# Optimization experiments

Measured on AMD Instinct MI355X. Metric: run time of the kernel, lower is better.

The kernel has to match this reference:

```python
import jax, jax.numpy as jnp
import numpy as np

D_MODEL = 1024
NUM_HEADS = 16
HEAD_DIM = D_MODEL // NUM_HEADS


def setup_inputs() -> dict:
    key = jax.random.key(0)
    ks = jax.random.split(key, 11)
    B, N = 2, 2048
    s = 1.0 / np.sqrt(D_MODEL)
    return {
        "query": jax.random.normal(ks[0], (B, N, D_MODEL), jnp.float32),
        "key":   jax.random.normal(ks[1], (B, N, D_MODEL), jnp.float32),
        "value": jax.random.normal(ks[2], (B, N, D_MODEL), jnp.float32),
        "Wq": jax.random.normal(ks[3], (D_MODEL, D_MODEL), jnp.float32) * s,
        "bq": jax.random.normal(ks[4], (D_MODEL,), jnp.float32) * 0.01,
        "Wk": jax.random.normal(ks[5], (D_MODEL, D_MODEL), jnp.float32) * s,
        "bk": jax.random.normal(ks[6], (D_MODEL,), jnp.float32) * 0.01,
        "Wv": jax.random.normal(ks[7], (D_MODEL, D_MODEL), jnp.float32) * s,
        "bv": jax.random.normal(ks[8], (D_MODEL,), jnp.float32) * 0.01,
        "Wo": jax.random.normal(ks[9], (D_MODEL, D_MODEL), jnp.float32) * s,
        "bo": jax.random.normal(ks[10], (D_MODEL,), jnp.float32) * 0.01,
    }


def _split_heads(x):
    # [B, N, d_model] -> [B, H, N, head_dim]
    B, N, _ = x.shape
    return x.reshape(B, N, NUM_HEADS, HEAD_DIM).transpose(0, 2, 1, 3)


def reference(query, key, value, Wq, bq, Wk, bk, Wv, bv, Wo, bo):
    B, N, _ = query.shape
    q = _split_heads(query @ Wq.T + bq)  # [B,H,N,dh]
    k = _split_heads(key @ Wk.T + bk)
    v = _split_heads(value @ Wv.T + bv)
    # NOTE: faithful to source: no 1/sqrt(head_dim) scaling.
    scores = jnp.einsum("bhnd,bhmd->bhnm", q, k)
    attn = jax.nn.softmax(scores, axis=-1)
    out = jnp.einsum("bhnm,bhmd->bhnd", attn, v)
    out = out.transpose(0, 2, 1, 3).reshape(B, N, D_MODEL)
    return out @ Wo.T + bo
```

## Files before the change

kernel.cpp:

```cpp
#include <hip/hip_runtime.h>
#include <cstdint>

#define DEV __device__ __forceinline__

typedef __bf16 bf16x8 __attribute__((ext_vector_type(8)));
typedef short s16x8 __attribute__((ext_vector_type(8)));
typedef float f32x4 __attribute__((ext_vector_type(4)));
typedef unsigned short u16;

constexpr int D_MODEL = 1024;
constexpr int SEQ = 2048;
constexpr float LOG2E = 1.4426950408889634f;
constexpr float SHIFT = 64.0f;

DEV u16 f2bf(float f) {
  uint32_t u = __float_as_uint(f);
  u += 0x7fff + ((u >> 16) & 1);
  return (u16)(u >> 16);
}

DEV void load_lds16(const void* g, void* l) {
  __builtin_amdgcn_global_load_lds((const __attribute__((address_space(1))) void*)g,
                                   (__attribute__((address_space(3))) void*)l, 16, 0, 0);
}

struct ConvArgs {
  const float* src[7];
  u16* dst[7];
  int n[7];
};

__global__ __launch_bounds__(256) void convert_kernel(ConvArgs a) {
  const int t = blockIdx.y;
  const int i = (blockIdx.x * 256 + threadIdx.x) * 4;
  if (i >= a.n[t]) return;
  const float4 v = *(const float4*)(a.src[t] + i);
  ushort4 o;
  o.x = f2bf(v.x); o.y = f2bf(v.y); o.z = f2bf(v.z); o.w = f2bf(v.w);
  *(ushort4*)(a.dst[t] + i) = o;
}

struct GemmArgs {
  const u16* A[3];
  const u16* W[3];
  const float* bias[3];
  u16* out[3];
  float scale[3];
};

__global__ __launch_bounds__(256, 2) void gemm_qkv(GemmArgs args) {
  __shared__ u16 lds[2][2][128 * 64];
  const int bid = blockIdx.x;
  const int xcd = bid & 7, j = bid >> 3;
  const int z = j >> 5;
  const int r0 = j & 31;
  const int m0 = (xcd * 4 + (r0 >> 3)) * 128;
  const int n0 = (r0 & 7) * 128;
  const u16* __restrict__ A = args.A[z];
  const u16* __restrict__ W = args.W[z];
  const int tid = threadIdx.x;
  const int lane = tid & 63, wid = tid >> 6;
  const int quad = lane >> 4, l16 = lane & 15;
  const int wm = wid >> 1, wn = wid & 1;

  f32x4 acc[4][4] = {};

#define GSTAGE(T, B)                                                              \
  {                                                                               \
    _Pragma("unroll")                                                             \
    for (int p = 0; p < 4; ++p) {                                                 \
      int c = p * 256 + tid;                                                      \
      int row = c >> 3;                                                           \
      int g = ((c & 7) ^ (row & 7)) * 8;                                          \
      load_lds16(A + (size_t)(m0 + row) * D_MODEL + (T) * 64 + g, &lds[B][0][c * 8]); \
      load_lds16(W + (size_t)(n0 + row) * D_MODEL + (T) * 64 + g, &lds[B][1][c * 8]); \
    }                                                                             \
  }

  GSTAGE(0, 0);
  __syncthreads();

  for (int kt = 0; kt < 16; ++kt) {
    if (kt + 1 < 16) GSTAGE(kt + 1, (kt + 1) & 1);
    const u16* lA = lds[kt & 1][0];
    const u16* lB = lds[kt & 1][1];
#pragma unroll
    for (int ks = 0; ks < 2; ++ks) {
      bf16x8 af[4], bfr[4];
#pragma unroll
      for (int mt = 0; mt < 4; ++mt) {
        int r = wm * 64 + mt * 16 + l16;
        int ch = (ks * 4 + quad) ^ (r & 7);
        af[mt] = *(const bf16x8*)&lA[r * 64 + ch * 8];
      }
#pragma unroll
      for (int nt = 0; nt < 4; ++nt) {
        int r = wn * 64 + nt * 16 + l16;
        int ch = (ks * 4 + quad) ^ (r & 7);
        bfr[nt] = *(const bf16x8*)&lB[r * 64 + ch * 8];
      }
#pragma unroll
      for (int mt = 0; mt < 4; ++mt)
#pragma unroll
        for (int nt = 0; nt < 4; ++nt)
          acc[mt][nt] = __builtin_amdgcn_mfma_f32_16x16x32_bf16(af[mt], bfr[nt], acc[mt][nt], 0, 0, 0);
    }
    __syncthreads();
  }
#undef GSTAGE

  const float* __restrict__ bias = args.bias[z];
  u16* out = args.out[z];
  float sc = args.scale[z];
#pragma unroll
  for (int nt = 0; nt < 4; ++nt) {
    int col = n0 + wn * 64 + nt * 16 + l16;
    float bv = bias[col];
    int h = col >> 6, d = col & 63;
#pragma unroll
    for (int mt = 0; mt < 4; ++mt) {
      int mb = m0 + wm * 64 + mt * 16 + quad * 4;
#pragma unroll
      for (int r = 0; r < 4; ++r) {
        int tok = mb + r;
        int b = tok >> 11, tt = tok & 2047;
        out[(((size_t)(b * 16 + h) * SEQ + tt) << 6) + d] = f2bf((acc[mt][nt][r] + bv) * sc);
      }
    }
  }
}

__global__ __launch_bounds__(256, 2) void gemm_out(const u16* __restrict__ A,
                                                   const u16* __restrict__ W,
                                                   const float* __restrict__ bias,
                                                   float* __restrict__ out) {
  __shared__ u16 lds[2][(128 + 64) * 64];
  const int bid = blockIdx.x;
  const int xcd = bid & 7, j = bid >> 3;
  const int m0 = (xcd * 4 + (j >> 4)) * 128;
  const int n0 = (j & 15) * 64;
  const int tid = threadIdx.x;
  const int lane = tid & 63, wid = tid >> 6;
  const int quad = lane >> 4, l16 = lane & 15;
  const int wm = wid >> 1, wn = wid & 1;

  f32x4 acc[4][2] = {};

#define OSTAGE(T, B)                                                              \
  {                                                                               \
    _Pragma("unroll")                                                             \
    for (int p = 0; p < 4; ++p) {                                                 \
      int c = p * 256 + tid;                                                      \
      int row = c >> 3;                                                           \
      int g = ((c & 7) ^ (row & 7)) * 8;                                          \
      load_lds16(A + (size_t)(m0 + row) * D_MODEL + (T) * 64 + g, &lds[B][c * 8]); \
    }                                                                             \
    _Pragma("unroll")                                                             \
    for (int p = 0; p < 2; ++p) {                                                 \
      int c = p * 256 + tid;                                                      \
      int row = c >> 3;                                                           \
      int g = ((c & 7) ^ (row & 7)) * 8;                                          \
      load_lds16(W + (size_t)(n0 + row) * D_MODEL + (T) * 64 + g,                 \
                 &lds[B][128 * 64 + c * 8]);                                      \
    }                                                                             \
  }

  OSTAGE(0, 0);
  __syncthreads();

  for (int kt = 0; kt < 16; ++kt) {
    if (kt + 1 < 16) OSTAGE(kt + 1, (kt + 1) & 1);
    const u16* lA = lds[kt & 1];
    const u16* lW = lds[kt & 1] + 128 * 64;
#pragma unroll
    for (int ks = 0; ks < 2; ++ks) {
      bf16x8 af[4], wf[2];
#pragma unroll
      for (int mt = 0; mt < 4; ++mt) {
        int r = wm * 64 + mt * 16 + l16;
        int ch = (ks * 4 + quad) ^ (r & 7);
        af[mt] = *(const bf16x8*)&lA[r * 64 + ch * 8];
      }
#pragma unroll
      for (int nt = 0; nt < 2; ++nt) {
        int r = wn * 32 + nt * 16 + l16;
        int ch = (ks * 4 + quad) ^ (r & 7);
        wf[nt] = *(const bf16x8*)&lW[r * 64 + ch * 8];
      }
#pragma unroll
      for (int mt = 0; mt < 4; ++mt)
#pragma unroll
        for (int nt = 0; nt < 2; ++nt)
          acc[mt][nt] = __builtin_amdgcn_mfma_f32_16x16x32_bf16(af[mt], wf[nt], acc[mt][nt], 0, 0, 0);
    }
    __syncthreads();
  }
#undef OSTAGE

#pragma unroll
  for (int nt = 0; nt < 2; ++nt) {
    int col = n0 + wn * 32 + nt * 16 + l16;
    float bv = bias[col];
#pragma unroll
    for (int mt = 0; mt < 4; ++mt) {
      int mb = m0 + wm * 64 + mt * 16 + quad * 4;
#pragma unroll
      for (int r = 0; r < 4; ++r)
        out[(size_t)(mb + r) * D_MODEL + col] = acc[mt][nt][r] + bv;
    }
  }
}

__global__ __launch_bounds__(256) void transpose_v(const u16* __restrict__ V, u16* __restrict__ Vt) {
  __shared__ u16 tile[64][66];
  const int bh = blockIdx.y;
  const int t0 = blockIdx.x * 64;
  const int tid = threadIdx.x;
  const u16* src = V + ((size_t)bh * SEQ + t0) * 64;
#pragma unroll
  for (int p = 0; p < 4; ++p) {
    int v = p * 256 + tid;
    int row = v >> 4, c4 = (v & 15) * 4;
    ushort4 x = *(const ushort4*)(src + (size_t)row * 64 + c4);
    tile[row][c4] = x.x; tile[row][c4 + 1] = x.y; tile[row][c4 + 2] = x.z; tile[row][c4 + 3] = x.w;
  }
  __syncthreads();
  u16* dst = Vt + (size_t)bh * 64 * SEQ + t0;
#pragma unroll
  for (int p = 0; p < 4; ++p) {
    int v = p * 256 + tid;
    int d = v >> 4, c4 = (v & 15) * 4;
    ushort4 o;
    o.x = tile[c4][d]; o.y = tile[c4 + 1][d]; o.z = tile[c4 + 2][d]; o.w = tile[c4 + 3][d];
    *(ushort4*)(dst + (size_t)d * SEQ + c4) = o;
  }
}

__global__ __launch_bounds__(256, 4) void attn_kernel(const u16* __restrict__ Q,
                                                      const u16* __restrict__ K,
                                                      const u16* __restrict__ Vt,
                                                      u16* __restrict__ O) {
  __shared__ u16 sm[2][2][64 * 64];
  const int bid = blockIdx.x;
  const int xcd = bid & 7, jj = bid >> 3;
  const int bh = xcd + 8 * (jj >> 5);
  const int q0 = (jj & 31) * 64;
  const int tid = threadIdx.x;
  const int lane = tid & 63, w = tid >> 6;
  const int quad = lane >> 4, l16 = lane & 15;
  const int kb = w & 1;
  const int pair = w >> 1;

  const u16* kbase = K + (size_t)bh * SEQ * 64;
  const u16* vtbase = Vt + (size_t)bh * 64 * SEQ;

  bf16x8 qf[2][2];
#pragma unroll
  for (int qh = 0; qh < 2; ++qh) {
    const u16* qrow = Q + ((size_t)bh * SEQ + q0 + pair * 32 + qh * 16 + l16) * 64;
    qf[qh][0] = *(const bf16x8*)(qrow + quad * 8);
    qf[qh][1] = *(const bf16x8*)(qrow + 32 + quad * 8);
  }

  bf16x8 onesA;
  {
    __bf16 v = (l16 == 0) ? (__bf16)1.0f : (__bf16)0.0f;
#pragma unroll
    for (int j = 0; j < 8; ++j) onesA[j] = v;
  }

  f32x4 acc[2][5] = {};
  const f32x4 minit = {-SHIFT, -SHIFT, -SHIFT, -SHIFT};

#define STAGE(T, B)                                                               \
  {                                                                               \
    _Pragma("unroll")                                                             \
    for (int p = 0; p < 2; ++p) {                                                 \
      int c = p * 256 + tid;                                                      \
      int row = c >> 3;                                                           \
      int km = (row & 32) | (((row >> 2) & 3) << 3) | (((row >> 4) & 1) << 2) |   \
               (row & 3);                                                         \
      int g = ((c & 7) ^ (row & 7)) * 8;                                          \
      load_lds16(kbase + (size_t)((T) * 64 + km) * 64 + g, &sm[B][0][c * 8]);     \
      load_lds16(vtbase + (size_t)row * SEQ + (T) * 64 + g, &sm[B][1][c * 8]);    \
    }                                                                             \
  }

  STAGE(0, 0);
  __syncthreads();

  for (int t = 0; t < SEQ / 64; ++t) {
    if (t + 1 < SEQ / 64) STAGE(t + 1, (t + 1) & 1);
    const u16* lK = sm[t & 1][0];
    const u16* lV = sm[t & 1][1];

    bf16x8 kf[2][2];
#pragma unroll
    for (int nt = 0; nt < 2; ++nt) {
      int r = kb * 32 + nt * 16 + l16;
#pragma unroll
      for (int ks = 0; ks < 2; ++ks) {
        int ch = (ks * 4 + quad) ^ (r & 7);
        kf[nt][ks] = *(const bf16x8*)&lK[r * 64 + ch * 8];
      }
    }

    s16x8 pf[2];
#pragma unroll
    for (int qh = 0; qh < 2; ++qh) {
      f32x4 s0 = __builtin_amdgcn_mfma_f32_16x16x32_bf16(kf[0][0], qf[qh][0], minit, 0, 0, 0);
      s0 = __builtin_amdgcn_mfma_f32_16x16x32_bf16(kf[0][1], qf[qh][1], s0, 0, 0, 0);
      f32x4 s1 = __builtin_amdgcn_mfma_f32_16x16x32_bf16(kf[1][0], qf[qh][0], minit, 0, 0, 0);
      s1 = __builtin_amdgcn_mfma_f32_16x16x32_bf16(kf[1][1], qf[qh][1], s1, 0, 0, 0);
      bf16x8 pb;
#pragma unroll
      for (int r = 0; r < 4; ++r) {
        pb[r] = (__bf16)__builtin_amdgcn_exp2f(s0[r]);
        pb[4 + r] = (__bf16)__builtin_amdgcn_exp2f(s1[r]);
      }
      pf[qh] = __builtin_bit_cast(s16x8, pb);
    }

#pragma unroll
    for (int dt = 0; dt < 4; ++dt) {
      int row = dt * 16 + l16;
      int ch = (kb * 4 + quad) ^ (row & 7);
      bf16x8 vf = *(const bf16x8*)&lV[row * 64 + ch * 8];
#pragma unroll
      for (int qh = 0; qh < 2; ++qh)
        acc[qh][dt] = __builtin_amdgcn_mfma_f32_16x16x32_bf16(
            vf, __builtin_bit_cast(bf16x8, pf[qh]), acc[qh][dt], 0, 0, 0);
    }
#pragma unroll
    for (int qh = 0; qh < 2; ++qh)
      acc[qh][4] = __builtin_amdgcn_mfma_f32_16x16x32_bf16(
          onesA, __builtin_bit_cast(bf16x8, pf[qh]), acc[qh][4], 0, 0, 0);

    __syncthreads();
  }
#undef STAGE

  float* red = (float*)&sm[0][0][0];
  if (kb == 1) {
#pragma unroll
    for (int qh = 0; qh < 2; ++qh)
#pragma unroll
      for (int dt = 0; dt < 5; ++dt)
        *(f32x4*)&red[(((pair * 2 + qh) * 5 + dt) * 64 + lane) * 4] = acc[qh][dt];
  }
  __syncthreads();
  if (kb == 0) {
    const int b = bh >> 4, h = bh & 15;
#pragma unroll
    for (int qh = 0; qh < 2; ++qh) {
#pragma unroll
      for (int dt = 0; dt < 5; ++dt)
        acc[qh][dt] += *(const f32x4*)&red[(((pair * 2 + qh) * 5 + dt) * 64 + lane) * 4];
      float sum = __shfl(acc[qh][4][0], l16, 64);
      float inv = 1.0f / sum;
      const int tok = b * SEQ + q0 + pair * 32 + qh * 16 + l16;
      u16* obase = O + (size_t)tok * D_MODEL + h * 64;
#pragma unroll
      for (int dt = 0; dt < 4; ++dt) {
        ushort4 o;
        o.x = f2bf(acc[qh][dt][0] * inv);
        o.y = f2bf(acc[qh][dt][1] * inv);
        o.z = f2bf(acc[qh][dt][2] * inv);
        o.w = f2bf(acc[qh][dt][3] * inv);
        *(ushort4*)(obase + dt * 16 + quad * 4) = o;
      }
    }
  }
}

extern "C" void kernel_launch(void* const* d_in, const int* in_sizes, int n_in,
                              void* d_out, int out_size, void* d_ws, size_t ws_size,
                              hipStream_t stream) {
  const float* q  = (const float*)d_in[0];
  const float* k  = (const float*)d_in[1];
  const float* v  = (const float*)d_in[2];
  const float* Wq = (const float*)d_in[3];
  const float* bq = (const float*)d_in[4];
  const float* Wk = (const float*)d_in[5];
  const float* bk = (const float*)d_in[6];
  const float* Wv = (const float*)d_in[7];
  const float* bv = (const float*)d_in[8];
  const float* Wo = (const float*)d_in[9];
  const float* bo = (const float*)d_in[10];

  uint8_t* ws = (uint8_t*)d_ws;
  const size_t MB = 1024 * 1024;
  u16* Xq  = (u16*)(ws + 0 * MB);
  u16* Xk  = (u16*)(ws + 8 * MB);
  u16* Xv  = (u16*)(ws + 16 * MB);
  u16* Wqb = (u16*)(ws + 24 * MB);
  u16* Wkb = (u16*)(ws + 26 * MB);
  u16* Wvb = (u16*)(ws + 28 * MB);
  u16* Wob = (u16*)(ws + 30 * MB);
  u16* Qb  = (u16*)(ws + 32 * MB);
  u16* Kb  = (u16*)(ws + 40 * MB);
  u16* Vb  = (u16*)(ws + 48 * MB);
  u16* Vtb = Xk;
  u16* Ob  = Xq;

  ConvArgs ca;
  ca.src[0] = q;  ca.dst[0] = Xq;  ca.n[0] = 4194304;
  ca.src[1] = k;  ca.dst[1] = Xk;  ca.n[1] = 4194304;
  ca.src[2] = v;  ca.dst[2] = Xv;  ca.n[2] = 4194304;
  ca.src[3] = Wq; ca.dst[3] = Wqb; ca.n[3] = 1048576;
  ca.src[4] = Wk; ca.dst[4] = Wkb; ca.n[4] = 1048576;
  ca.src[5] = Wv; ca.dst[5] = Wvb; ca.n[5] = 1048576;
  ca.src[6] = Wo; ca.dst[6] = Wob; ca.n[6] = 1048576;
  convert_kernel<<<dim3(4096, 7), 256, 0, stream>>>(ca);

  GemmArgs ga;
  ga.A[0] = Xq; ga.A[1] = Xk; ga.A[2] = Xv;
  ga.W[0] = Wqb; ga.W[1] = Wkb; ga.W[2] = Wvb;
  ga.bias[0] = bq; ga.bias[1] = bk; ga.bias[2] = bv;
  ga.out[0] = Qb; ga.out[1] = Kb; ga.out[2] = Vb;
  ga.scale[0] = LOG2E; ga.scale[1] = 1.0f; ga.scale[2] = 1.0f;
  gemm_qkv<<<dim3(768), 256, 0, stream>>>(ga);

  transpose_v<<<dim3(32, 32), 256, 0, stream>>>(Vb, Vtb);

  attn_kernel<<<dim3(1024), 256, 0, stream>>>(Qb, Kb, Vtb, Ob);

  gemm_out<<<dim3(512), 256, 0, stream>>>(Ob, Wob, bo, (float*)d_out);
}
```

Before: 212.9 us.

## Write V transposed from QKV GEMM epilogue and read V fragments directly from global

The QKV projection epilogue now writes V directly in [bh, d, token] layout using 4-wide stores, so the separate transpose_v kernel and its extra round trip through memory are removed. The attention kernel stops staging V through LDS and instead loads each V fragment straight from global memory into registers at the start of each tile. LDS use drops to K only. s_setprio is raised around the MFMA groups. The direct global V reads depend on cache hits and on being issued early enough to hide their latency.

```diff
diff --git a/kernel.cpp b/kernel.cpp
--- a/kernel.cpp
+++ b/kernel.cpp
@@ -112,19 +112,39 @@
   const float* __restrict__ bias = args.bias[z];
   u16* out = args.out[z];
   float sc = args.scale[z];
-#pragma unroll
-  for (int nt = 0; nt < 4; ++nt) {
-    int col = n0 + wn * 64 + nt * 16 + l16;
-    float bv = bias[col];
-    int h = col >> 6, d = col & 63;
-#pragma unroll
-    for (int mt = 0; mt < 4; ++mt) {
-      int mb = m0 + wm * 64 + mt * 16 + quad * 4;
-#pragma unroll
-      for (int r = 0; r < 4; ++r) {
-        int tok = mb + r;
-        int b = tok >> 11, tt = tok & 2047;
-        out[(((size_t)(b * 16 + h) * SEQ + tt) << 6) + d] = f2bf((acc[mt][nt][r] + bv) * sc);
+  if (z == 2) {
+#pragma unroll
+    for (int nt = 0; nt < 4; ++nt) {
+      int col = n0 + wn * 64 + nt * 16 + l16;
+      float bv = bias[col];
+      int h = col >> 6, d = col & 63;
+#pragma unroll
+      for (int mt = 0; mt < 4; ++mt) {
+        int mb = m0 + wm * 64 + mt * 16 + quad * 4;
+        int b = mb >> 11, tt = mb & 2047;
+        ushort4 o;
+        o.x = f2bf(acc[mt][nt][0] + bv);
+        o.y = f2bf(acc[mt][nt][1] + bv);
+        o.z = f2bf(acc[mt][nt][2] + bv);
+        o.w = f2bf(acc[mt][nt][3] + bv);
+        *(ushort4*)(out + ((size_t)(b * 16 + h) * 64 + d) * SEQ + tt) = o;
+      }
+    }
+  } else {
+#pragma unroll
+    for (int nt = 0; nt < 4; ++nt) {
+      int col = n0 + wn * 64 + nt * 16 + l16;
+      float bv = bias[col];
+      int h = col >> 6, d = col & 63;
+#pragma unroll
+      for (int mt = 0; mt < 4; ++mt) {
+        int mb = m0 + wm * 64 + mt * 16 + quad * 4;
+#pragma unroll
+        for (int r = 0; r < 4; ++r) {
+          int tok = mb + r;
+          int b = tok >> 11, tt = tok & 2047;
+          out[(((size_t)(b * 16 + h) * SEQ + tt) << 6) + d] = f2bf((acc[mt][nt][r] + bv) * sc);
+        }
       }
     }
   }
@@ -211,36 +231,12 @@
   }
 }
 
-__global__ __launch_bounds__(256) void transpose_v(const u16* __restrict__ V, u16* __restrict__ Vt) {
-  __shared__ u16 tile[64][66];
-  const int bh = blockIdx.y;
-  const int t0 = blockIdx.x * 64;
-  const int tid = threadIdx.x;
-  const u16* src = V + ((size_t)bh * SEQ + t0) * 64;
-#pragma unroll
-  for (int p = 0; p < 4; ++p) {
-    int v = p * 256 + tid;
-    int row = v >> 4, c4 = (v & 15) * 4;
-    ushort4 x = *(const ushort4*)(src + (size_t)row * 64 + c4);
-    tile[row][c4] = x.x; tile[row][c4 + 1] = x.y; tile[row][c4 + 2] = x.z; tile[row][c4 + 3] = x.w;
-  }
-  __syncthreads();
-  u16* dst = Vt + (size_t)bh * 64 * SEQ + t0;
-#pragma unroll
-  for (int p = 0; p < 4; ++p) {
-    int v = p * 256 + tid;
-    int d = v >> 4, c4 = (v & 15) * 4;
-    ushort4 o;
-    o.x = tile[c4][d]; o.y = tile[c4 + 1][d]; o.z = tile[c4 + 2][d]; o.w = tile[c4 + 3][d];
-    *(ushort4*)(dst + (size_t)d * SEQ + c4) = o;
-  }
-}
-
 __global__ __launch_bounds__(256, 4) void attn_kernel(const u16* __restrict__ Q,
                                                       const u16* __restrict__ K,
                                                       const u16* __restrict__ Vt,
                                                       u16* __restrict__ O) {
-  __shared__ u16 sm[2][2][64 * 64];
+  __shared__ uint8_t smraw[20480];
+  u16* smK = (u16*)smraw;
   const int bid = blockIdx.x;
   const int xcd = bid & 7, jj = bid >> 3;
   const int bh = xcd + 8 * (jj >> 5);
@@ -262,6 +258,11 @@
     qf[qh][1] = *(const bf16x8*)(qrow + 32 + quad * 8);
   }
 
+  const u16* vp[4];
+#pragma unroll
+  for (int dt = 0; dt < 4; ++dt)
+    vp[dt] = vtbase + (size_t)(dt * 16 + l16) * SEQ + kb * 32 + quad * 8;
+
   bf16x8 onesA;
   {
     __bf16 v = (l16 == 0) ? (__bf16)1.0f : (__bf16)0.0f;
@@ -281,8 +282,7 @@
       int km = (row & 32) | (((row >> 2) & 3) << 3) | (((row >> 4) & 1) << 2) |   \
                (row & 3);                                                         \
       int g = ((c & 7) ^ (row & 7)) * 8;                                          \
-      load_lds16(kbase + (size_t)((T) * 64 + km) * 64 + g, &sm[B][0][c * 8]);     \
-      load_lds16(vtbase + (size_t)row * SEQ + (T) * 64 + g, &sm[B][1][c * 8]);    \
+      load_lds16(kbase + (size_t)((T) * 64 + km) * 64 + g, &smK[(B) * 4096 + c * 8]); \
     }                                                                             \
   }
 
@@ -290,9 +290,13 @@
   __syncthreads();
 
   for (int t = 0; t < SEQ / 64; ++t) {
+    bf16x8 vf[4];
+#pragma unroll
+    for (int dt = 0; dt < 4; ++dt)
+      vf[dt] = *(const bf16x8*)(vp[dt] + t * 64);
+
     if (t + 1 < SEQ / 64) STAGE(t + 1, (t + 1) & 1);
-    const u16* lK = sm[t & 1][0];
-    const u16* lV = sm[t & 1][1];
+    const u16* lK = smK + (t & 1) * 4096;
 
     bf16x8 kf[2][2];
 #pragma unroll
@@ -305,42 +309,47 @@
       }
     }
 
+    f32x4 s[2][2];
+    __builtin_amdgcn_s_setprio(1);
+#pragma unroll
+    for (int qh = 0; qh < 2; ++qh) {
+      s[qh][0] = __builtin_amdgcn_mfma_f32_16x16x32_bf16(kf[0][0], qf[qh][0], minit, 0, 0, 0);
+      s[qh][0] = __builtin_amdgcn_mfma_f32_16x16x32_bf16(kf[0][1], qf[qh][1], s[qh][0], 0, 0, 0);
+      s[qh][1] = __builtin_amdgcn_mfma_f32_16x16x32_bf16(kf[1][0], qf[qh][0], minit, 0, 0, 0);
+      s[qh][1] = __builtin_amdgcn_mfma_f32_16x16x32_bf16(kf[1][1], qf[qh][1], s[qh][1], 0, 0, 0);
+    }
+    __builtin_amdgcn_s_setprio(0);
+
     s16x8 pf[2];
 #pragma unroll
     for (int qh = 0; qh < 2; ++qh) {
-      f32x4 s0 = __builtin_amdgcn_mfma_f32_16x16x32_bf16(kf[0][0], qf[qh][0], minit, 0, 0, 0);
-      s0 = __builtin_amdgcn_mfma_f32_16x16x32_bf16(kf[0][1], qf[qh][1], s0, 0, 0, 0);
-      f32x4 s1 = __builtin_amdgcn_mfma_f32_16x16x32_bf16(kf[1][0], qf[qh][0], minit, 0, 0, 0);
-      s1 = __builtin_amdgcn_mfma_f32_16x16x32_bf16(kf[1][1], qf[qh][1], s1, 0, 0, 0);
       bf16x8 pb;
 #pragma unroll
       for (int r = 0; r < 4; ++r) {
-        pb[r] = (__bf16)__builtin_amdgcn_exp2f(s0[r]);
-        pb[4 + r] = (__bf16)__builtin_amdgcn_exp2f(s1[r]);
+        pb[r] = (__bf16)__builtin_amdgcn_exp2f(s[qh][0][r]);
+        pb[4 + r] = (__bf16)__builtin_amdgcn_exp2f(s[qh][1][r]);
       }
       pf[qh] = __builtin_bit_cast(s16x8, pb);
     }
 
-#pragma unroll
-    for (int dt = 0; dt < 4; ++dt) {
-      int row = dt * 16 + l16;
-      int ch = (kb * 4 + quad) ^ (row & 7);
-      bf16x8 vf = *(const bf16x8*)&lV[row * 64 + ch * 8];
+    __builtin_amdgcn_s_setprio(1);
+#pragma unroll
+    for (int dt = 0; dt < 4; ++dt)
 #pragma unroll
       for (int qh = 0; qh < 2; ++qh)
         acc[qh][dt] = __builtin_amdgcn_mfma_f32_16x16x32_bf16(
-            vf, __builtin_bit_cast(bf16x8, pf[qh]), acc[qh][dt], 0, 0, 0);
-    }
+            vf[dt], __builtin_bit_cast(bf16x8, pf[qh]), acc[qh][dt], 0, 0, 0);
 #pragma unroll
     for (int qh = 0; qh < 2; ++qh)
       acc[qh][4] = __builtin_amdgcn_mfma_f32_16x16x32_bf16(
           onesA, __builtin_bit_cast(bf16x8, pf[qh]), acc[qh][4], 0, 0, 0);
+    __builtin_amdgcn_s_setprio(0);
 
     __syncthreads();
   }
 #undef STAGE
 
-  float* red = (float*)&sm[0][0][0];
+  float* red = (float*)smraw;
   if (kb == 1) {
 #pragma unroll
     for (int qh = 0; qh < 2; ++qh)
@@ -399,8 +408,7 @@
   u16* Wob = (u16*)(ws + 30 * MB);
   u16* Qb  = (u16*)(ws + 32 * MB);
   u16* Kb  = (u16*)(ws + 40 * MB);
-  u16* Vb  = (u16*)(ws + 48 * MB);
-  u16* Vtb = Xk;
+  u16* Vtb = (u16*)(ws + 48 * MB);
   u16* Ob  = Xq;
 
   ConvArgs ca;
@@ -417,12 +425,10 @@
   ga.A[0] = Xq; ga.A[1] = Xk; ga.A[2] = Xv;
   ga.W[0] = Wqb; ga.W[1] = Wkb; ga.W[2] = Wvb;
   ga.bias[0] = bq; ga.bias[1] = bk; ga.bias[2] = bv;
-  ga.out[0] = Qb; ga.out[1] = Kb; ga.out[2] = Vb;
+  ga.out[0] = Qb; ga.out[1] = Kb; ga.out[2] = Vtb;
   ga.scale[0] = LOG2E; ga.scale[1] = 1.0f; ga.scale[2] = 1.0f;
   gemm_qkv<<<dim3(768), 256, 0, stream>>>(ga);
 
-  transpose_v<<<dim3(32, 32), 256, 0, stream>>>(Vb, Vtb);
-
   attn_kernel<<<dim3(1024), 256, 0, stream>>>(Qb, Kb, Vtb, Ob);
 
   gemm_out<<<dim3(512), 256, 0, stream>>>(Ob, Wob, bo, (float*)d_out);
```

Result: slower. 242.5 us (+13.9%).
